# Performance work log

Hardware: AMD Instinct MI355X
Metric: run time of the kernel (lower is better)

Reference implementation:

```python
import jax, jax.numpy as jnp
import numpy as np

B, S, L, H, D, DF = 2, 1024, 2, 8, 512, 2048
DK = D // H  # head dim (dk == dv == 64)
EPS = 1e-5


def _ln(x, g, b):
    m = jnp.mean(x, axis=-1, keepdims=True)
    v = jnp.mean((x - m) ** 2, axis=-1, keepdims=True)
    return (x - m) / jnp.sqrt(v + EPS) * g + b


def setup_inputs() -> dict:
    key = jax.random.key(0)
    ks = jax.random.split(key, 8)
    sd = 1.0 / np.sqrt(D)
    sf = 1.0 / np.sqrt(DF)
    inp = {
        "src": jax.random.normal(ks[0], (B, S, D), jnp.float32),
        "Wq": jax.random.normal(ks[1], (L, D, D), jnp.float32) * sd,
        "bq": jnp.zeros((L, D), jnp.float32),
        "Wk": jax.random.normal(ks[2], (L, D, D), jnp.float32) * sd,
        "bk": jnp.zeros((L, D), jnp.float32),
        "Wv": jax.random.normal(ks[3], (L, D, D), jnp.float32) * sd,
        "bv": jnp.zeros((L, D), jnp.float32),
        "Wo": jax.random.normal(ks[4], (L, D, D), jnp.float32) * sd,
        "bo": jnp.zeros((L, D), jnp.float32),
        "W1": jax.random.normal(ks[5], (L, D, DF), jnp.float32) * sd,
        "b1": jnp.zeros((L, DF), jnp.float32),
        "W2": jax.random.normal(ks[6], (L, DF, D), jnp.float32) * sf,
        "b2": jnp.zeros((L, D), jnp.float32),
        "g1": jnp.ones((L, D), jnp.float32),
        "be1": jnp.zeros((L, D), jnp.float32),
        "g2": jnp.ones((L, D), jnp.float32),
        "be2": jnp.zeros((L, D), jnp.float32),
        "gf": jnp.ones((D,), jnp.float32),
        "bef": jnp.zeros((D,), jnp.float32),
    }
    return inp


def _heads(x):
    # [B,S,D] -> [B,H,S,DK]
    return x.reshape(B, S, H, DK).transpose(0, 2, 1, 3)


def _causal_linear_attention(q, k, v):
    # Faithful to torch: cumsum of per-step KV outer products, then query contraction.
    kv = jnp.einsum("bhsk,bhsv->bhskv", k, v)      # [B,H,S,DK,DK]
    cum = jnp.cumsum(kv, axis=2)                     # prefix sums over sequence
    return jnp.einsum("bhsk,bhskv->bhsv", q, cum)   # [B,H,S,DK]


def reference(src, Wq, bq, Wk, bk, Wv, bv, Wo, bo, W1, b1, W2, b2,
              g1, be1, g2, be2, gf, bef):
    x = src
    for i in range(L):
        q = _heads(x @ Wq[i] + bq[i])
        k = _heads(x @ Wk[i] + bk[i])
        v = _heads(x @ Wv[i] + bv[i])
        att = _causal_linear_attention(q, k, v)
        att = att.transpose(0, 2, 1, 3).reshape(B, S, D)
        att = att @ Wo[i] + bo[i]
        x = _ln(x + att, g1[i], be1[i])              # post-norm (normalize_before=False)
        ff = jax.nn.relu(x @ W1[i] + b1[i]) @ W2[i] + b2[i]
        x = _ln(x + ff, g2[i], be2[i])
    return _ln(x, gf, bef)                            # final encoder LayerNorm
```

## Files before the change

### kernel.cpp

```cpp
#include <hip/hip_runtime.h>
#include <hip/hip_bf16.h>

#define DEV static __device__ __forceinline__

typedef __attribute__((ext_vector_type(8))) short short8;
typedef __attribute__((ext_vector_type(4))) float f32x4;

DEV unsigned short f2b(float f){
  unsigned int u = __float_as_uint(f);
  return (unsigned short)((u + 0x7FFFu + ((u >> 16) & 1u)) >> 16);
}
DEV float b2f(unsigned short h){ return __uint_as_float(((unsigned int)h) << 16); }
DEV float load_in(const void* p, size_t i, int isbf){
  return isbf ? b2f(((const unsigned short*)p)[i]) : ((const float*)p)[i];
}
DEV void load_lds16(const unsigned short* g, unsigned short* l){
  __builtin_amdgcn_global_load_lds(
      (const __attribute__((address_space(1))) void*)g,
      (__attribute__((address_space(3))) void*)l, 16, 0, 0);
}

DEV int detect_isbf_block(const void* src){
  __shared__ int cnt[4];
  int tid = threadIdx.x;
  float v = b2f(((const unsigned short*)src)[2 * tid]);
  float av = fabsf(v);
  bool sane = ((av < 64.0f) && (av > 9.5e-7f)) || (v == 0.0f);
  unsigned long long m = __ballot(sane);
  if ((tid & 63) == 0) cnt[tid >> 6] = __popcll(m);
  __syncthreads();
  int tot = cnt[0] + cnt[1] + cnt[2] + cnt[3];
  __syncthreads();
  return tot > 128;
}

struct WDesc { const void* src; long src_off; unsigned short* dst; int K; int N; int tstart; };
struct WParams { WDesc d[12]; const void* dsrc; };

__global__ __launch_bounds__(256) void ingest_weights(WParams P){
  __shared__ float tile[32][33];
  int isbf = detect_isbf_block(P.dsrc);
  int b = blockIdx.x;
  int t = 0;
  #pragma unroll
  for (int i = 1; i < 12; ++i) if (b >= P.d[i].tstart) t = i;
  WDesc d = P.d[t];
  int r = b - d.tstart;
  int tiles_x = d.N >> 5;
  int tx = r % tiles_x, ty = r / tiles_x;
  int lx = threadIdx.x & 31, ly = threadIdx.x >> 5;
  #pragma unroll
  for (int i = 0; i < 4; ++i){
    int row = ty*32 + ly + i*8;
    int col = tx*32 + lx;
    tile[ly + i*8][lx] = load_in(d.src, (size_t)d.src_off + (size_t)row*d.N + col, isbf);
  }
  __syncthreads();
  #pragma unroll
  for (int i = 0; i < 4; ++i){
    int orow = tx*32 + ly + i*8;
    int ocol = ty*32 + lx;
    d.dst[(size_t)orow*d.K + ocol] = f2b(tile[lx][ly + i*8]);
  }
}

struct SDesc { const void* src; int src_off; int dstart; };
struct SParams { SDesc d[22]; float* dst; int total; };

__global__ __launch_bounds__(256) void ingest_misc(SParams S, const void* src,
                                                   float* xf, unsigned short* xb){
  int isbf = detect_isbf_block(src);
  int b = blockIdx.x, tid = threadIdx.x;
  if (b < 4096){
    int i = b*256 + tid;
    float v = load_in(src, (size_t)i, isbf);
    xf[i] = v; xb[i] = f2b(v);
  } else {
    int i = (b - 4096)*256 + tid;
    if (i < S.total){
      int t = 0;
      #pragma unroll
      for (int j = 1; j < 22; ++j) if (i >= S.d[j].dstart) t = j;
      S.dst[i] = load_in(S.d[t].src, (size_t)S.d[t].src_off + (i - S.d[t].dstart), isbf);
    }
  }
}

struct GemmArgs {
  const unsigned short* A;
  const unsigned short* Bt;
  const float* bias;
  float* Cf;
  unsigned short* Cb;
  int K;
  int lda, ldb, ldc;
  int cshift, cmask;
  size_t cstride;
  size_t cfz;
  int relu;
};

template<int BN>
__global__ __launch_bounds__(256) void gemm_bt(GemmArgs g){
  constexpr int NI = (BN == 128) ? 4 : 2;
  constexpr int NJ = 4;
  constexpr int BPASS = BN / 32;
  __shared__ __align__(16) unsigned short sA[128*64];
  __shared__ __align__(16) unsigned short sB[BN*64];
  int tid = threadIdx.x;
  int koff = blockIdx.z * g.K;
  int K = g.K, lda = g.lda, ldb = g.ldb;
  size_t bm = (size_t)blockIdx.y * 128, bn = (size_t)blockIdx.x * BN;
  int lane = tid & 63, wv = tid >> 6, quad = lane >> 4, l16 = lane & 15;
  int wm = (BN == 128) ? (wv >> 1) * 64 : wv * 32;
  int wn = (BN == 128) ? (wv & 1) * 64 : 0;
  f32x4 acc[NI][NJ];
  #pragma unroll
  for (int i=0;i<NI;++i)
    #pragma unroll
    for (int j=0;j<NJ;++j) acc[i][j] = (f32x4){0.f,0.f,0.f,0.f};
  int srow = tid >> 3;
  int schunk = (tid & 7) ^ (srow & 7);
  const unsigned short* Ap = g.A  + (bm + srow)*lda + koff + schunk*8;
  const unsigned short* Bp = g.Bt + (bn + srow)*ldb + koff + schunk*8;
  for (int ko = 0; ko < K; ko += 64){
    __syncthreads();
    #pragma unroll
    for (int p = 0; p < 4; ++p)
      load_lds16(Ap + (size_t)(p*32)*lda + ko, &sA[p*2048 + tid*8]);
    #pragma unroll
    for (int p = 0; p < BPASS; ++p)
      load_lds16(Bp + (size_t)(p*32)*ldb + ko, &sB[p*2048 + tid*8]);
    __syncthreads();
    #pragma unroll
    for (int kk = 0; kk < 2; ++kk){
      short8 af[NI], bfv[NJ];
      #pragma unroll
      for (int i=0;i<NI;++i){
        int row = wm + i*16 + l16;
        int ch  = (kk*4 + quad) ^ (row & 7);
        af[i] = *(const short8*)&sA[row*64 + ch*8];
      }
      #pragma unroll
      for (int j=0;j<NJ;++j){
        int row = wn + j*16 + l16;
        int ch  = (kk*4 + quad) ^ (row & 7);
        bfv[j] = *(const short8*)&sB[row*64 + ch*8];
      }
      #pragma unroll
      for (int i=0;i<NI;++i)
        #pragma unroll
        for (int j=0;j<NJ;++j)
          acc[i][j] = __builtin_amdgcn_mfma_f32_16x16x32_bf16(af[i], bfv[j], acc[i][j], 0,0,0);
    }
  }
  float* Cf = g.Cf ? g.Cf + (size_t)blockIdx.z * g.cfz : nullptr;
  unsigned short* Cb = g.Cb;
  #pragma unroll
  for (int j=0;j<NJ;++j){
    int col = (int)bn + wn + j*16 + l16;
    float bv = g.bias ? g.bias[col] : 0.f;
    size_t cbase = ((size_t)(col >> g.cshift))*g.cstride + (col & g.cmask);
    #pragma unroll
    for (int i=0;i<NI;++i){
      #pragma unroll
      for (int r=0;r<4;++r){
        int row = (int)bm + wm + i*16 + quad*4 + r;
        float v = acc[i][j][r] + bv;
        if (g.relu) v = fmaxf(v, 0.f);
        size_t idx = cbase + (size_t)row*g.ldc;
        if (Cf) Cf[idx] = v;
        if (Cb) Cb[idx] = f2b(v);
      }
    }
  }
}

#define ATT_S 1024
#define ATT_D 512

__global__ __launch_bounds__(256) void attn_state_kernel(
    const unsigned short* k, const unsigned short* v, float* states)
{
  __shared__ __align__(16) unsigned short sVt[64*72];
  __shared__ __align__(16) unsigned short sKt[64*72];
  int tid = threadIdx.x;
  int c = blockIdx.x, bh = blockIdx.y;
  int b = bh >> 3, h = bh & 7;
  const size_t base = ((size_t)b*ATT_S + (size_t)c*64)*ATT_D + h*64;
  int lane = tid & 63, wv = tid >> 6, quad = lane >> 4, l16 = lane & 15;

  int t = lane, vc = wv*8;
  const unsigned short* vp = v + base + (size_t)t*ATT_D;
  const unsigned short* kp = k + base + (size_t)t*ATT_D;
  float4 v0 = *(const float4*)(vp + vc);
  float4 v1 = *(const float4*)(vp + vc + 32);
  float4 k0 = *(const float4*)(kp + vc);
  float4 k1 = *(const float4*)(kp + vc + 32);
  {
    const unsigned short* pv0 = (const unsigned short*)&v0;
    const unsigned short* pv1 = (const unsigned short*)&v1;
    const unsigned short* pk0 = (const unsigned short*)&k0;
    const unsigned short* pk1 = (const unsigned short*)&k1;
    #pragma unroll
    for (int e = 0; e < 8; ++e){
      sVt[(vc+e)*72 + t]    = pv0[e];
      sVt[(vc+32+e)*72 + t] = pv1[e];
      sKt[(vc+e)*72 + t]    = pk0[e];
      sKt[(vc+32+e)*72 + t] = pk1[e];
    }
  }
  __syncthreads();

  f32x4 acc[4];
  #pragma unroll
  for (int j=0;j<4;++j) acc[j] = (f32x4){0.f,0.f,0.f,0.f};
  #pragma unroll
  for (int kk=0;kk<2;++kk){
    short8 a = *(const short8*)&sVt[(wv*16 + l16)*72 + kk*32 + quad*8];
    #pragma unroll
    for (int j=0;j<4;++j){
      short8 bb = *(const short8*)&sKt[(j*16 + l16)*72 + kk*32 + quad*8];
      acc[j] = __builtin_amdgcn_mfma_f32_16x16x32_bf16(a, bb, acc[j], 0,0,0);
    }
  }
  float* st = states + ((size_t)bh*16 + c)*4096;
  #pragma unroll
  for (int j=0;j<4;++j)
    #pragma unroll
    for (int rr=0;rr<4;++rr)
      st[(wv*16 + quad*4 + rr)*64 + j*16 + l16] = acc[j][rr];
}

__global__ __launch_bounds__(256) void attn_out_kernel(
    const unsigned short* q, const unsigned short* k, const unsigned short* v,
    const float* states, unsigned short* att)
{
  __shared__ __align__(16) unsigned short sQ [64*72];
  __shared__ __align__(16) unsigned short sK [64*72];
  __shared__ __align__(16) unsigned short sVt[64*72];
  __shared__ __align__(16) float sKV[64*68];
  int tid = threadIdx.x;
  int c = blockIdx.x, bh = blockIdx.y;
  int b = bh >> 3, h = bh & 7;
  const size_t base = ((size_t)b*ATT_S + (size_t)c*64)*ATT_D + h*64;
  int lane = tid & 63, wv = tid >> 6, quad = lane >> 4, l16 = lane & 15;

  float4 racc[4];
  #pragma unroll
  for (int u=0;u<4;++u) racc[u] = (float4){0.f,0.f,0.f,0.f};
  const float* sbase = states + (size_t)bh*16*4096;
  for (int cc = 0; cc < c; ++cc){
    const float4* sp = (const float4*)(sbase + (size_t)cc*4096);
    #pragma unroll
    for (int u=0;u<4;++u){
      float4 t4 = sp[tid + u*256];
      racc[u].x += t4.x; racc[u].y += t4.y; racc[u].z += t4.z; racc[u].w += t4.w;
    }
  }
  #pragma unroll
  for (int u=0;u<4;++u){
    int e = (tid + u*256)*4;
    int row = e >> 6, col = e & 63;
    *(float4*)&sKV[row*68 + col] = racc[u];
  }

  int r = tid >> 2, c8 = (tid & 3)*8;
  const unsigned short* qp = q + base + (size_t)r*ATT_D;
  const unsigned short* kp = k + base + (size_t)r*ATT_D;
  float4 q0 = *(const float4*)(qp + c8);
  float4 q1 = *(const float4*)(qp + c8 + 32);
  float4 k0 = *(const float4*)(kp + c8);
  float4 k1 = *(const float4*)(kp + c8 + 32);
  int t = lane, vc = wv*8;
  const unsigned short* vp = v + base + (size_t)t*ATT_D;
  float4 v0 = *(const float4*)(vp + vc);
  float4 v1 = *(const float4*)(vp + vc + 32);
  *(float4*)&sQ[r*72 + c8]      = q0;
  *(float4*)&sQ[r*72 + c8 + 32] = q1;
  *(float4*)&sK[r*72 + c8]      = k0;
  *(float4*)&sK[r*72 + c8 + 32] = k1;
  {
    const unsigned short* pv0 = (const unsigned short*)&v0;
    const unsigned short* pv1 = (const unsigned short*)&v1;
    #pragma unroll
    for (int e=0;e<8;++e){
      sVt[(vc+e)*72 + t]    = pv0[e];
      sVt[(vc+32+e)*72 + t] = pv1[e];
    }
  }
  __syncthreads();

  f32x4 accS[4];
  #pragma unroll
  for (int j=0;j<4;++j) accS[j] = (f32x4){0.f,0.f,0.f,0.f};
  #pragma unroll
  for (int kk=0;kk<2;++kk){
    short8 a = *(const short8*)&sQ[(wv*16 + l16)*72 + kk*32 + quad*8];
    #pragma unroll
    for (int j=0;j<4;++j){
      short8 bb = *(const short8*)&sK[(j*16 + l16)*72 + kk*32 + quad*8];
      accS[j] = __builtin_amdgcn_mfma_f32_16x16x32_bf16(a, bb, accS[j], 0,0,0);
    }
  }
  __syncthreads();

  #pragma unroll
  for (int j=0;j<4;++j)
    #pragma unroll
    for (int rr=0;rr<4;++rr){
      int i  = wv*16 + quad*4 + rr;
      int cj = j*16 + l16;
      sK[i*72 + cj] = f2b((i >= cj) ? accS[j][rr] : 0.f);
    }

  f32x4 accO[4];
  #pragma unroll
  for (int j=0;j<4;++j) accO[j] = (f32x4){0.f,0.f,0.f,0.f};
  #pragma unroll
  for (int kk=0;kk<2;++kk){
    short8 a = *(const short8*)&sQ[(wv*16 + l16)*72 + kk*32 + quad*8];
    #pragma unroll
    for (int j=0;j<4;++j){
      const float* pf = &sKV[(j*16 + l16)*68 + kk*32 + quad*8];
      short8 bb;
      #pragma unroll
      for (int e=0;e<8;++e) ((unsigned short*)&bb)[e] = f2b(pf[e]);
      accO[j] = __builtin_amdgcn_mfma_f32_16x16x32_bf16(a, bb, accO[j], 0,0,0);
    }
  }
  __syncthreads();

  #pragma unroll
  for (int kk=0;kk<2;++kk){
    short8 a = *(const short8*)&sK[(wv*16 + l16)*72 + kk*32 + quad*8];
    #pragma unroll
    for (int j=0;j<4;++j){
      short8 bb = *(const short8*)&sVt[(j*16 + l16)*72 + kk*32 + quad*8];
      accO[j] = __builtin_amdgcn_mfma_f32_16x16x32_bf16(a, bb, accO[j], 0,0,0);
    }
  }
  #pragma unroll
  for (int j=0;j<4;++j)
    #pragma unroll
    for (int rr=0;rr<4;++rr){
      int i  = wv*16 + quad*4 + rr;
      int cj = j*16 + l16;
      att[base + (size_t)i*ATT_D + cj] = f2b(accO[j][rr]);
    }
}

__global__ __launch_bounds__(256) void add_ln_kernel(
    const float* x, const float* p, int np, const float* bias,
    const float* g, const float* bta,
    float* outf, unsigned short* outb, void* outd, const void* dsrc, int rows)
{
  int isbf = 0;
  if (dsrc) isbf = detect_isbf_block(dsrc);
  int row = blockIdx.x*4 + (threadIdx.x >> 6);
  int lane = threadIdx.x & 63;
  if (row >= rows) return;
  const float* xr = x + (size_t)row*512;
  float a[8];
  *(float4*)&a[0] = *(const float4*)(xr + lane*4);
  *(float4*)&a[4] = *(const float4*)(xr + 256 + lane*4);
  for (int s = 0; s < np; ++s){
    const float* pr = p + (size_t)s*1048576 + (size_t)row*512;
    float yb[8];
    *(float4*)&yb[0] = *(const float4*)(pr + lane*4);
    *(float4*)&yb[4] = *(const float4*)(pr + 256 + lane*4);
    #pragma unroll
    for (int e=0;e<8;++e) a[e] += yb[e];
  }
  if (bias){
    float bb2[8];
    *(float4*)&bb2[0] = *(const float4*)(bias + lane*4);
    *(float4*)&bb2[4] = *(const float4*)(bias + 256 + lane*4);
    #pragma unroll
    for (int e=0;e<8;++e) a[e] += bb2[e];
  }
  float s = 0.f, qq = 0.f;
  #pragma unroll
  for (int e=0;e<8;++e){ s += a[e]; qq += a[e]*a[e]; }
  #pragma unroll
  for (int off=32; off>0; off>>=1){
    s  += __shfl_xor(s,  off, 64);
    qq += __shfl_xor(qq, off, 64);
  }
  float mean = s * (1.f/512.f);
  float var  = qq * (1.f/512.f) - mean*mean;
  float rstd = rsqrtf(var + 1e-5f);
  float gg[8], bb[8];
  *(float4*)&gg[0] = *(const float4*)(g + lane*4);
  *(float4*)&gg[4] = *(const float4*)(g + 256 + lane*4);
  *(float4*)&bb[0] = *(const float4*)(bta + lane*4);
  *(float4*)&bb[4] = *(const float4*)(bta + 256 + lane*4);
  #pragma unroll
  for (int e=0;e<8;++e) a[e] = (a[e]-mean)*rstd*gg[e] + bb[e];
  if (outf){
    float* orow = outf + (size_t)row*512;
    *(float4*)(orow + lane*4)       = *(float4*)&a[0];
    *(float4*)(orow + 256 + lane*4) = *(float4*)&a[4];
  }
  if (outb){
    unsigned short* orow = outb + (size_t)row*512;
    #pragma unroll
    for (int e=0;e<4;++e){ orow[lane*4+e] = f2b(a[e]); orow[256+lane*4+e] = f2b(a[4+e]); }
  }
  if (outd){
    if (isbf){
      unsigned short* od = (unsigned short*)outd + (size_t)row*512;
      #pragma unroll
      for (int e=0;e<4;++e){ od[lane*4+e] = f2b(a[e]); od[256+lane*4+e] = f2b(a[4+e]); }
    } else {
      float* od = (float*)outd + (size_t)row*512;
      *(float4*)(od + lane*4)       = *(float4*)&a[0];
      *(float4*)(od + 256 + lane*4) = *(float4*)&a[4];
    }
  }
}

extern "C" void kernel_launch(void* const* d_in, const int* in_sizes, int n_in,
                              void* d_out, int out_size, void* d_ws, size_t ws_size,
                              hipStream_t stream)
{
  (void)in_sizes; (void)n_in; (void)out_size; (void)ws_size;
  const void* src = d_in[0];
  const void* Wq = d_in[1];  const void* bq = d_in[2];
  const void* Wk = d_in[3];  const void* bk = d_in[4];
  const void* Wv = d_in[5];  const void* bv = d_in[6];
  const void* Wo = d_in[7];  const void* bo = d_in[8];
  const void* W1 = d_in[9];  const void* b1 = d_in[10];
  const void* W2 = d_in[11]; const void* b2 = d_in[12];
  const void* g1 = d_in[13]; const void* be1 = d_in[14];
  const void* g2 = d_in[15]; const void* be2 = d_in[16];
  const void* gf = d_in[17]; const void* bef = d_in[18];

  char* W = (char*)d_ws;
  float* smalls          = (float*)(W + 256);
  unsigned short* wt     = (unsigned short*)(W + 65536);
  float* x_f             = (float*)(W + 12648448);
  unsigned short* x_b    = (unsigned short*)(W + 16842752);
  unsigned short* q_b    = (unsigned short*)(W + 18939904);
  unsigned short* att_b  = (unsigned short*)(W + 25231360);
  float* pp              = (float*)(W + 27328512);
  unsigned short* h1_b   = (unsigned short*)(W + 44105728);
  float* states          = (float*)(W + 44105728);
  unsigned short* k_b = q_b + 1048576;
  unsigned short* v_b = q_b + 2097152;

  WParams wp;
  {
    const void* wsrc[6] = {Wq, Wk, Wv, Wo, W1, W2};
    int wK[6] = {512,512,512,512,512,2048};
    int wN[6] = {512,512,512,512,2048,512};
    long wsz[6] = {262144,262144,262144,262144,1048576,1048576};
    int tstart = 0; size_t dsto = 0;
    for (int l=0;l<2;++l)
      for (int ti=0;ti<6;++ti){
        int idx = l*6+ti;
        wp.d[idx].src = wsrc[ti];
        wp.d[idx].src_off = (long)l * wsz[ti];
        wp.d[idx].dst = wt + dsto;
        wp.d[idx].K = wK[ti]; wp.d[idx].N = wN[ti];
        wp.d[idx].tstart = tstart;
        tstart += (wK[ti]/32)*(wN[ti]/32);
        dsto += (size_t)wsz[ti];
      }
    wp.dsrc = src;
    ingest_weights<<<dim3(6144), 256, 0, stream>>>(wp);
  }

  SParams sp;
  {
    const void* ss[10] = {bq,bk,bv,bo,b1,b2,g1,be1,g2,be2};
    int slen[10] = {512,512,512,512,2048,512,512,512,512,512};
    int dcur = 0, di = 0;
    for (int l=0;l<2;++l)
      for (int ti=0;ti<10;++ti){
        sp.d[di].src = ss[ti];
        sp.d[di].src_off = l * slen[ti];
        sp.d[di].dstart = dcur;
        dcur += slen[ti]; ++di;
      }
    sp.d[20].src = gf;  sp.d[20].src_off = 0; sp.d[20].dstart = dcur; dcur += 512;
    sp.d[21].src = bef; sp.d[21].src_off = 0; sp.d[21].dstart = dcur; dcur += 512;
    sp.dst = smalls; sp.total = dcur;
    ingest_misc<<<dim3(4152), 256, 0, stream>>>(sp, src, x_f, x_b);
  }

  for (int l = 0; l < 2; ++l){
    unsigned short* WqkvT = wt + (size_t)l*3145728;
    unsigned short* WoT   = WqkvT + 786432;
    unsigned short* W1T   = WqkvT + 1048576;
    unsigned short* W2T   = WqkvT + 2097152;
    float* base  = smalls + l*6656;
    float* p_bqkv= base;
    float* p_bo  = base + 1536;
    float* p_b1  = base + 2048;
    float* p_b2  = base + 4096;
    float* p_g1  = base + 4608;
    float* p_be1 = base + 5120;
    float* p_g2  = base + 5632;
    float* p_be2 = base + 6144;

    GemmArgs qkv = {};
    qkv.A = x_b; qkv.Bt = WqkvT; qkv.bias = p_bqkv;
    qkv.Cf = nullptr; qkv.Cb = q_b;
    qkv.K = 512; qkv.lda = 512; qkv.ldb = 512; qkv.ldc = 512;
    qkv.cshift = 9; qkv.cmask = 511; qkv.cstride = 1048576; qkv.cfz = 0; qkv.relu = 0;
    gemm_bt<64><<<dim3(24,16,1), 256, 0, stream>>>(qkv);

    attn_state_kernel<<<dim3(16,16), 256, 0, stream>>>(k_b, v_b, states);
    attn_out_kernel<<<dim3(16,16), 256, 0, stream>>>(q_b, k_b, v_b, states, att_b);

    GemmArgs go = {};
    go.A = att_b; go.Bt = WoT; go.bias = nullptr;
    go.Cf = pp; go.Cb = nullptr;
    go.K = 256; go.lda = 512; go.ldb = 512; go.ldc = 512;
    go.cshift = 30; go.cmask = 0x3fffffff; go.cstride = 0; go.cfz = 1048576; go.relu = 0;
    gemm_bt<64><<<dim3(8,16,2), 256, 0, stream>>>(go);

    add_ln_kernel<<<dim3(512), 256, 0, stream>>>(x_f, pp, 2, p_bo, p_g1, p_be1,
                                                 x_f, x_b, nullptr, nullptr, 2048);

    GemmArgs f1 = {};
    f1.A = x_b; f1.Bt = W1T; f1.bias = p_b1;
    f1.Cf = nullptr; f1.Cb = h1_b;
    f1.K = 512; f1.lda = 512; f1.ldb = 512; f1.ldc = 2048;
    f1.cshift = 30; f1.cmask = 0x3fffffff; f1.cstride = 0; f1.cfz = 0; f1.relu = 1;
    gemm_bt<128><<<dim3(16,16,1), 256, 0, stream>>>(f1);

    GemmArgs f2 = {};
    f2.A = h1_b; f2.Bt = W2T; f2.bias = nullptr;
    f2.Cf = pp; f2.Cb = nullptr;
    f2.K = 512; f2.lda = 2048; f2.ldb = 2048; f2.ldc = 512;
    f2.cshift = 30; f2.cmask = 0x3fffffff; f2.cstride = 0; f2.cfz = 1048576; f2.relu = 0;
    gemm_bt<64><<<dim3(8,16,4), 256, 0, stream>>>(f2);

    add_ln_kernel<<<dim3(512), 256, 0, stream>>>(x_f, pp, 4, p_b2, p_g2, p_be2,
                                                 x_f, x_b, nullptr, nullptr, 2048);
  }

  add_ln_kernel<<<dim3(512), 256, 0, stream>>>(x_f, nullptr, 0, nullptr,
                                               smalls + 13312, smalls + 13824,
                                               nullptr, nullptr, d_out, src, 2048);
}
```

Baseline: 267.4 us.

## Double-buffer LDS tiles in GEMM to overlap global loads with MFMA

Doubles the shared-memory A/B tile buffers in the bt GEMM. The next K tile is prefetched via global_load_lds while the current one feeds MFMAs, with one waitcnt plus barrier per iteration instead of two barriers. This is meant to hide global-to-LDS latency. It doubles LDS use per block, which can lower occupancy.

```diff
diff --git a/kernel.cpp b/kernel.cpp
--- a/kernel.cpp
+++ b/kernel.cpp
@@ -105,8 +105,8 @@
   constexpr int NI = (BN == 128) ? 4 : 2;
   constexpr int NJ = 4;
   constexpr int BPASS = BN / 32;
-  __shared__ __align__(16) unsigned short sA[128*64];
-  __shared__ __align__(16) unsigned short sB[BN*64];
+  __shared__ __align__(16) unsigned short sA[2][128*64];
+  __shared__ __align__(16) unsigned short sB[2][BN*64];
   int tid = threadIdx.x;
   int koff = blockIdx.z * g.K;
   int K = g.K, lda = g.lda, ldb = g.ldb;
@@ -123,15 +123,28 @@
   int schunk = (tid & 7) ^ (srow & 7);
   const unsigned short* Ap = g.A  + (bm + srow)*lda + koff + schunk*8;
   const unsigned short* Bp = g.Bt + (bn + srow)*ldb + koff + schunk*8;
-  for (int ko = 0; ko < K; ko += 64){
-    __syncthreads();
-    #pragma unroll
-    for (int p = 0; p < 4; ++p)
-      load_lds16(Ap + (size_t)(p*32)*lda + ko, &sA[p*2048 + tid*8]);
-    #pragma unroll
-    for (int p = 0; p < BPASS; ++p)
-      load_lds16(Bp + (size_t)(p*32)*ldb + ko, &sB[p*2048 + tid*8]);
-    __syncthreads();
+
+  #define STAGE(buf, ko)                                                      \
+    do {                                                                      \
+      _Pragma("unroll")                                                       \
+      for (int p = 0; p < 4; ++p)                                             \
+        load_lds16(Ap + (size_t)(p*32)*lda + (ko), &sA[buf][p*2048 + tid*8]); \
+      _Pragma("unroll")                                                       \
+      for (int p = 0; p < BPASS; ++p)                                         \
+        load_lds16(Bp + (size_t)(p*32)*ldb + (ko), &sB[buf][p*2048 + tid*8]); \
+    } while (0)
+
+  STAGE(0, 0);
+  asm volatile("s_waitcnt vmcnt(0)" ::: "memory");
+  __builtin_amdgcn_s_barrier();
+
+  int nt = K >> 6;
+  int cur = 0;
+  for (int t = 0; t < nt; ++t){
+    if (t + 1 < nt){
+      STAGE(cur ^ 1, (t + 1) * 64);
+      __builtin_amdgcn_sched_barrier(0);
+    }
     #pragma unroll
     for (int kk = 0; kk < 2; ++kk){
       short8 af[NI], bfv[NJ];
@@ -139,13 +152,13 @@
       for (int i=0;i<NI;++i){
         int row = wm + i*16 + l16;
         int ch  = (kk*4 + quad) ^ (row & 7);
-        af[i] = *(const short8*)&sA[row*64 + ch*8];
+        af[i] = *(const short8*)&sA[cur][row*64 + ch*8];
       }
       #pragma unroll
       for (int j=0;j<NJ;++j){
         int row = wn + j*16 + l16;
         int ch  = (kk*4 + quad) ^ (row & 7);
-        bfv[j] = *(const short8*)&sB[row*64 + ch*8];
+        bfv[j] = *(const short8*)&sB[cur][row*64 + ch*8];
       }
       #pragma unroll
       for (int i=0;i<NI;++i)
@@ -153,7 +166,14 @@
         for (int j=0;j<NJ;++j)
           acc[i][j] = __builtin_amdgcn_mfma_f32_16x16x32_bf16(af[i], bfv[j], acc[i][j], 0,0,0);
     }
-  }
+    if (t + 1 < nt){
+      asm volatile("s_waitcnt vmcnt(0)" ::: "memory");
+      __builtin_amdgcn_s_barrier();
+    }
+    cur ^= 1;
+  }
+  #undef STAGE
+
   float* Cf = g.Cf ? g.Cf + (size_t)blockIdx.z * g.cfz : nullptr;
   unsigned short* Cb = g.Cb;
   #pragma unroll
```

Measured after the change: 264.8 us. Within noise of the previous version (-1.0%).
